# Kernel optimization log

Measured on AMD Instinct MI355X. Metric: run time of the kernel, lower is better.

Reference implementation:

```python
import jax, jax.numpy as jnp
import numpy as np

B = 32768
PASSES = 4

# mask layout: (batch, digit, row, col), values in {0,1}

def _to_lines(m, d):
    """Reorder so the last axis enumerates the 9 cells of a line and axis -2 the 9 lines."""
    if d == 'h':
        return m                      # lines = rows, cells = cols
    if d == 'v':
        return jnp.swapaxes(m, 2, 3)  # lines = cols, cells = rows
    b = m.shape[0]                    # lines = 3x3 boxes
    return m.reshape(b, 9, 3, 3, 3, 3).transpose(0, 1, 2, 4, 3, 5).reshape(b, 9, 9, 9)

_from_lines = _to_lines  # all three reorderings are self-inverse


def filter_line(m, d):
    """SudokuFilterHVBox: remove a solved cell's digit from all other cells in its line."""
    l = _to_lines(m, d)
    cnt = l.sum(axis=1, keepdims=True)                 # candidates per cell
    solved = l * (cnt == 1).astype(l.dtype)            # one-hot solved cells
    other = solved.sum(axis=-1, keepdims=True) - solved  # same digit solved elsewhere in line
    out = l * (other == 0).astype(l.dtype)
    return _from_lines(out, d)


def unique_line(m, d):
    """SudokuUniqueHVBox (hidden single): if a digit fits only one cell in a line, fix it."""
    l = _to_lines(m, d)
    cnt_line = l.sum(axis=-1, keepdims=True)           # per-digit count in the line
    hidden = l * (cnt_line == 1).astype(l.dtype)       # lone placements
    has = hidden.sum(axis=1, keepdims=True) > 0        # cell hosts a hidden single
    out = jnp.where(has, hidden, l)
    return _from_lines(out, d)


def doubles_line(m, d):
    """SudokuDigitsDoubles (naked pair): two identical 2-candidate cells in a line
    eliminate those digits from the rest of the line."""
    l = _to_lines(m, d)                                # (B, d, line, cell)
    cnt = l.sum(axis=1, keepdims=True)
    pm = l * (cnt == 2).astype(l.dtype)                # patterns of 2-candidate cells
    dot = jnp.einsum('bdlc,bdle->blce', pm, pm)        # pattern overlap between cells
    eye = jnp.eye(9, dtype=l.dtype)
    match = (dot == 2).astype(l.dtype) * (1.0 - eye)   # identical pair at another cell
    pairflag = match.sum(-1) > 0                       # (B, line, cell) part of a naked pair
    pair_digit = pm * pairflag[:, None, :, :].astype(l.dtype)
    total_pd = pair_digit.sum(-1, keepdims=True)       # digit belongs to some pair in line
    remove = (total_pd > 0) & (pair_digit == 0)
    out = l * (1.0 - remove.astype(l.dtype))
    return _from_lines(out, d)


def pointing(m, d):
    """SudokuDigitsInOneLineAtBox: if a digit's box candidates lie in one row/col,
    remove that digit from the rest of the row/col outside the box."""
    b = m.shape[0]
    v = m.reshape(b, 9, 3, 3, 3, 3)                    # (B, d, br, ri, bc, ci)
    if d == 'h':
        pres = v.sum(axis=5) > 0                       # (B,d,br,ri,bc) digit in row of box
        nrows = pres.sum(axis=3, keepdims=True)
        point = pres & (nrows == 1)                    # confined to single row within box
        tot = point.sum(axis=4, keepdims=True)         # over bc
        rem = (tot - point) > 0                        # pointing from another box hits us
        out = v * (1.0 - rem[..., None].astype(v.dtype))
    else:
        pres = v.sum(axis=3) > 0                       # (B,d,br,bc,ci) digit in col of box
        ncols = pres.sum(axis=4, keepdims=True)
        point = pres & (ncols == 1)
        tot = point.sum(axis=2, keepdims=True)         # over br
        rem = (tot - point) > 0
        out = v * (1.0 - rem[:, :, :, None, :, :].astype(v.dtype))
    return out.reshape(b, 9, 9, 9)


def _forward_mask(mask):
    for _ in range(PASSES):
        mask = filter_line(mask, 'box')
        mask = pointing(mask, 'h')
        mask = pointing(mask, 'v')
        mask = unique_line(mask, 'h')
        mask = unique_line(mask, 'v')
        mask = unique_line(mask, 'box')
        mask = doubles_line(mask, 'v')   # original code instantiates doubles_h with 'v'
        mask = doubles_line(mask, 'v')
        mask = doubles_line(mask, 'box')
    return mask


def setup_inputs() -> dict:
    key = jax.random.key(0)
    mask = jax.random.randint(key, (B, 9, 9, 9), 0, 2).astype(jnp.float32)
    return {"mask": mask}


def reference(mask):
    out = _forward_mask(mask)
    cnt = out.sum(axis=1)                              # candidates per cell
    solved = jnp.all(cnt == 1, axis=(1, 2))            # (B,) puzzle fully determined
    return (out, solved)
```

## Files before the change

### kernel.cpp

```cpp
#include <hip/hip_runtime.h>
#include <stdint.h>

#define NB 32768
#define NPASS 4
#define FULL27 0x07FFFFFFu
#define NWORDS (NB * 27)


__global__ __launch_bounds__(256)
void pack_kernel(const uint32_t* __restrict__ in, uint32_t* __restrict__ packed) {
    __shared__ uint32_t pool[4][56];
    const int lane = threadIdx.x & 63;
    const int wv = threadIdx.x >> 6;
    const size_t wordBase = (size_t)blockIdx.x * 256 + (size_t)wv * 64;
    const uint32_t* src = in + wordBase * 27;
    #pragma unroll
    for (int i = 0; i < 27; ++i) {
        uint32_t v = src[(size_t)i * 64 + lane];
        unsigned long long m = __ballot(v != 0u);
        if (lane == 0) {
            pool[wv][2 * i]     = (uint32_t)m;
            pool[wv][2 * i + 1] = (uint32_t)(m >> 32);
        }
    }
    __syncthreads();
    const int bit = lane * 27;
    const int di = bit >> 5;
    uint64_t both = (uint64_t)pool[wv][di] | ((uint64_t)pool[wv][di + 1] << 32);
    packed[wordBase + lane] = (uint32_t)(both >> (bit & 31)) & FULL27;
}

__global__ __launch_bounds__(256, 1)
void solve_kernel(const uint32_t* __restrict__ pin, uint32_t* __restrict__ pout,
                  float* __restrict__ solved) {
    int p = blockIdx.x * blockDim.x + threadIdx.x;
    if (p >= NB) return;
    uint32_t bd[9][3];
    {
        const uint32_t* src = pin + (size_t)p * 27;
        #pragma unroll
        for (int i = 0; i < 27; ++i) bd[i / 3][i % 3] = src[i];
    }

    #pragma unroll 1
    for (int pass = 0; pass < NPASS; ++pass) {
        {
            uint32_t on[3] = {0,0,0}, tw[3] = {0,0,0}, fo[3] = {0,0,0};
            #pragma unroll
            for (int d = 0; d < 9; ++d)
                #pragma unroll
                for (int b = 0; b < 3; ++b) {
                    uint32_t c = on[b] & bd[d][b];
                    on[b] ^= bd[d][b];
                    fo[b] |= tw[b] & c;
                    tw[b] ^= c;
                }
            uint32_t ex1[3];
            #pragma unroll
            for (int b = 0; b < 3; ++b) ex1[b] = on[b] & ~tw[b] & ~fo[b];
            #pragma unroll
            for (int d = 0; d < 9; ++d)
                #pragma unroll
                for (int b = 0; b < 3; ++b) {
                    uint32_t s = bd[d][b] & ex1[b];
                    #pragma unroll
                    for (int k = 0; k < 3; ++k) {
                        uint32_t bm = 0x1C0E07u << (3 * k);
                        uint32_t sm = s & bm;
                        uint32_t multi = sm & (sm - 1u);
                        uint32_t keep = (sm == 0u) ? 0xFFFFFFFFu : (~bm | (multi ? 0u : sm));
                        bd[d][b] &= keep;
                    }
                }
        }

        #pragma unroll
        for (int d = 0; d < 9; ++d)
            #pragma unroll
            for (int b = 0; b < 3; ++b) {
                uint32_t w = bd[d][b];
                uint32_t t = (w | (w >> 1) | (w >> 2)) & 0x01249249u;
                uint32_t sum = (t & 0x1FFu) + ((t >> 9) & 0x1FFu) + ((t >> 18) & 0x1FFu);
                uint32_t single = sum & ~(sum >> 1) & 0x49u;
                uint32_t point = t & (single * 0x40201u);
                uint32_t clearm = 0;
                #pragma unroll
                for (int r = 0; r < 3; ++r) {
                    uint32_t pr = (point >> (9 * r)) & 0x1FFu;
                    uint32_t multi = pr & (pr - 1u);
                    uint32_t segkeep = multi ? 0u : pr * 7u;
                    uint32_t rc = pr ? ((0x1FFu & ~segkeep) << (9 * r)) : 0u;
                    clearm |= rc;
                }
                bd[d][b] = w & ~clearm;
            }

        #pragma unroll
        for (int d = 0; d < 9; ++d) {
            uint32_t pnt[3];
            #pragma unroll
            for (int b = 0; b < 3; ++b) {
                uint32_t w = bd[d][b];
                uint32_t q = (w | (w >> 9) | (w >> 18)) & 0x1FFu;
                uint32_t u = (q & 0x49u) + ((q >> 1) & 0x49u) + ((q >> 2) & 0x49u);
                uint32_t single = u & ~(u >> 1) & 0x49u;
                pnt[b] = q & (single * 7u);
            }
            bd[d][0] &= ~((pnt[1] | pnt[2]) * 0x40201u);
            bd[d][1] &= ~((pnt[0] | pnt[2]) * 0x40201u);
            bd[d][2] &= ~((pnt[0] | pnt[1]) * 0x40201u);
        }

        {
            uint32_t hid[9][3];
            uint32_t has[3] = {0,0,0};
            #pragma unroll
            for (int d = 0; d < 9; ++d)
                #pragma unroll
                for (int b = 0; b < 3; ++b) {
                    uint32_t w = bd[d][b], h = 0;
                    #pragma unroll
                    for (int r = 0; r < 3; ++r) {
                        uint32_t x = w & (0x1FFu << (9 * r));
                        h |= (x & (x - 1u)) ? 0u : x;
                    }
                    hid[d][b] = h;
                    has[b] |= h;
                }
            #pragma unroll
            for (int d = 0; d < 9; ++d)
                #pragma unroll
                for (int b = 0; b < 3; ++b)
                    bd[d][b] = (bd[d][b] & ~has[b]) | hid[d][b];
        }

        {
            uint32_t hid[9][3];
            uint32_t has[3] = {0,0,0};
            #pragma unroll
            for (int d = 0; d < 9; ++d) {
                uint32_t h0 = 0, h1 = 0, h2 = 0;
                #pragma unroll
                for (int c = 0; c < 9; ++c) {
                    uint32_t cm = 0x40201u << c;
                    uint32_t a0 = bd[d][0] & cm;
                    uint32_t a1 = bd[d][1] & cm;
                    uint32_t a2 = bd[d][2] & cm;
                    uint32_t cnt = (uint32_t)(__popc(a0) + __popc(a1) + __popc(a2));
                    uint32_t mm = (cnt == 1u) ? 0xFFFFFFFFu : 0u;
                    h0 |= a0 & mm; h1 |= a1 & mm; h2 |= a2 & mm;
                }
                hid[d][0] = h0; hid[d][1] = h1; hid[d][2] = h2;
                has[0] |= h0; has[1] |= h1; has[2] |= h2;
            }
            #pragma unroll
            for (int d = 0; d < 9; ++d)
                #pragma unroll
                for (int b = 0; b < 3; ++b)
                    bd[d][b] = (bd[d][b] & ~has[b]) | hid[d][b];
        }

        {
            uint32_t hid[9][3];
            uint32_t has[3] = {0,0,0};
            #pragma unroll
            for (int d = 0; d < 9; ++d)
                #pragma unroll
                for (int b = 0; b < 3; ++b) {
                    uint32_t w = bd[d][b], h = 0;
                    #pragma unroll
                    for (int k = 0; k < 3; ++k) {
                        uint32_t x = w & (0x1C0E07u << (3 * k));
                        h |= (x & (x - 1u)) ? 0u : x;
                    }
                    hid[d][b] = h;
                    has[b] |= h;
                }
            #pragma unroll
            for (int d = 0; d < 9; ++d)
                #pragma unroll
                for (int b = 0; b < 3; ++b)
                    bd[d][b] = (bd[d][b] & ~has[b]) | hid[d][b];
        }

        #pragma unroll 1
        for (int rep = 0; rep < 2; ++rep) {
            uint32_t on[3] = {0,0,0}, tw[3] = {0,0,0}, fo[3] = {0,0,0};
            #pragma unroll
            for (int d = 0; d < 9; ++d)
                #pragma unroll
                for (int b = 0; b < 3; ++b) {
                    uint32_t c = on[b] & bd[d][b];
                    on[b] ^= bd[d][b];
                    fo[b] |= tw[b] & c;
                    tw[b] ^= c;
                }
            uint32_t ex2[3], Q[9][3], K[9][3];
            #pragma unroll
            for (int b = 0; b < 3; ++b) ex2[b] = tw[b] & ~on[b] & ~fo[b];
            #pragma unroll
            for (int d = 0; d < 9; ++d)
                #pragma unroll
                for (int b = 0; b < 3; ++b) { Q[d][b] = bd[d][b] & ex2[b]; K[d][b] = 0u; }
            #pragma unroll
            for (int d1 = 0; d1 < 9; ++d1)
                #pragma unroll
                for (int d2 = d1 + 1; d2 < 9; ++d2) {
                    uint32_t P0 = Q[d1][0] & Q[d2][0];
                    uint32_t P1 = Q[d1][1] & Q[d2][1];
                    uint32_t P2 = Q[d1][2] & Q[d2][2];
                    uint32_t f0 = (P0 | (P0 >> 9) | (P0 >> 18)) & 0x1FFu;
                    uint32_t f1 = (P1 | (P1 >> 9) | (P1 >> 18)) & 0x1FFu;
                    uint32_t f2 = (P2 | (P2 >> 9) | (P2 >> 18)) & 0x1FFu;
                    uint32_t g0 = ((P0 & (P0 >> 9)) | ((P0 | (P0 >> 9)) & (P0 >> 18))) & 0x1FFu;
                    uint32_t g1 = ((P1 & (P1 >> 9)) | ((P1 | (P1 >> 9)) & (P1 >> 18))) & 0x1FFu;
                    uint32_t g2 = ((P2 & (P2 >> 9)) | ((P2 | (P2 >> 9)) & (P2 >> 18))) & 0x1FFu;
                    uint32_t dup = g0 | g1 | g2 | (f0 & f1) | (f0 & f2) | (f1 & f2);
                    uint32_t em = dup * 0x40201u;
                    uint32_t s0 = P0 & em, s1 = P1 & em, s2 = P2 & em;
                    K[d1][0] |= s0; K[d1][1] |= s1; K[d1][2] |= s2;
                    K[d2][0] |= s0; K[d2][1] |= s1; K[d2][2] |= s2;
                }
            #pragma unroll
            for (int d = 0; d < 9; ++d) {
                uint32_t fold = K[d][0] | K[d][1] | K[d][2];
                uint32_t cols = (fold | (fold >> 9) | (fold >> 18)) & 0x1FFu;
                uint32_t em = cols * 0x40201u;
                #pragma unroll
                for (int b = 0; b < 3; ++b)
                    bd[d][b] = (bd[d][b] & ~em) | K[d][b];
            }
        }

        {
            uint32_t on[3] = {0,0,0}, tw[3] = {0,0,0}, fo[3] = {0,0,0};
            #pragma unroll
            for (int d = 0; d < 9; ++d)
                #pragma unroll
                for (int b = 0; b < 3; ++b) {
                    uint32_t c = on[b] & bd[d][b];
                    on[b] ^= bd[d][b];
                    fo[b] |= tw[b] & c;
                    tw[b] ^= c;
                }
            uint32_t ex2[3], Q[9][3], K[9][3];
            #pragma unroll
            for (int b = 0; b < 3; ++b) ex2[b] = tw[b] & ~on[b] & ~fo[b];
            #pragma unroll
            for (int d = 0; d < 9; ++d)
                #pragma unroll
                for (int b = 0; b < 3; ++b) { Q[d][b] = bd[d][b] & ex2[b]; K[d][b] = 0u; }
            #pragma unroll
            for (int d1 = 0; d1 < 9; ++d1)
                #pragma unroll
                for (int d2 = d1 + 1; d2 < 9; ++d2)
                    #pragma unroll
                    for (int b = 0; b < 3; ++b) {
                        uint32_t P = Q[d1][b] & Q[d2][b];
                        #pragma unroll
                        for (int k = 0; k < 3; ++k) {
                            uint32_t m = P & (0x1C0E07u << (3 * k));
                            uint32_t s = (m & (m - 1u)) ? m : 0u;
                            K[d1][b] |= s; K[d2][b] |= s;
                        }
                    }
            #pragma unroll
            for (int d = 0; d < 9; ++d)
                #pragma unroll
                for (int b = 0; b < 3; ++b)
                    #pragma unroll
                    for (int k = 0; k < 3; ++k) {
                        uint32_t bm = 0x1C0E07u << (3 * k);
                        uint32_t t = K[d][b] & bm;
                        uint32_t mask = t ? (~bm | t) : 0xFFFFFFFFu;
                        bd[d][b] &= mask;
                    }
        }
    }

    {
        uint32_t* dst = pout + (size_t)p * 27;
        #pragma unroll
        for (int i = 0; i < 27; ++i) dst[i] = bd[i / 3][i % 3];
    }
    {
        uint32_t on[3] = {0,0,0}, tw[3] = {0,0,0}, fo[3] = {0,0,0};
        #pragma unroll
        for (int d = 0; d < 9; ++d)
            #pragma unroll
            for (int b = 0; b < 3; ++b) {
                uint32_t c = on[b] & bd[d][b];
                on[b] ^= bd[d][b];
                fo[b] |= tw[b] & c;
                tw[b] ^= c;
            }
        bool ok = ((on[0] & ~tw[0] & ~fo[0]) == FULL27) &&
                  ((on[1] & ~tw[1] & ~fo[1]) == FULL27) &&
                  ((on[2] & ~tw[2] & ~fo[2]) == FULL27);
        solved[p] = ok ? 1.0f : 0.0f;
    }
}

__global__ __launch_bounds__(256)
void expand_kernel(const uint32_t* __restrict__ packed, float4* __restrict__ out4) {
    int tid = blockIdx.x * blockDim.x + threadIdx.x;
    int base = tid * 4;
    int w0 = (int)((unsigned)base / 27u);
    int pos0 = base - w0 * 27;
    uint32_t a = packed[w0];
    int w1 = w0 + 1; if (w1 > NWORDS - 1) w1 = NWORDS - 1;
    uint32_t b = packed[w1];
    float r[4];
    #pragma unroll
    for (int k = 0; k < 4; ++k) {
        int pp = pos0 + k;
        uint32_t word = (pp < 27) ? a : b;
        int sh = (pp < 27) ? pp : pp - 27;
        r[k] = (float)((word >> sh) & 1u);
    }
    out4[tid] = make_float4(r[0], r[1], r[2], r[3]);
}

extern "C" void kernel_launch(void* const* d_in, const int* in_sizes, int n_in,
                              void* d_out, int out_size, void* d_ws, size_t ws_size,
                              hipStream_t stream) {
    const uint32_t* in = (const uint32_t*)d_in[0];
    float* out = (float*)d_out;
    float* solved = out + (size_t)NB * 729;
    uint32_t* packed = (uint32_t*)d_ws;

    pack_kernel<<<NWORDS / 256, 256, 0, stream>>>(in, packed);
    solve_kernel<<<NB / 256, 256, 0, stream>>>(packed, packed, solved);
    expand_kernel<<<(NB * 729 / 4) / 256, 256, 0, stream>>>(packed, (float4*)out);
}
```

Before: 256.3 us.

## Split each puzzle across three threads by band with shared-memory exchange

The solve kernel now gives each puzzle to three threads, one per 3-row band, instead of one. Each thread holds 9 words instead of 27. Column-wise steps (column pointing, column hidden singles, column naked pairs, the solved check) exchange folded per-band summaries through shared memory with __syncthreads. This cuts register pressure and raises parallelism, since the old kernel had only 128 blocks of 256 threads. The cost is extra LDS traffic and block-wide barriers, about 30 KB of shared memory per block, and the same redundant colfold work repeated in each thread.

```diff
diff --git a/kernel.cpp b/kernel.cpp
--- a/kernel.cpp
+++ b/kernel.cpp
@@ -30,274 +30,250 @@
     packed[wordBase + lane] = (uint32_t)(both >> (bit & 31)) & FULL27;
 }
 
-__global__ __launch_bounds__(256, 1)
+__device__ __forceinline__ uint32_t colfold(uint32_t w) {
+    return (w | (w >> 9) | (w >> 18)) & 0x1FFu;
+}
+__device__ __forceinline__ uint32_t colmaj2(uint32_t w) {
+    return ((w & (w >> 9)) | ((w | (w >> 9)) & (w >> 18))) & 0x1FFu;
+}
+
+__global__ __launch_bounds__(192, 1)
 void solve_kernel(const uint32_t* __restrict__ pin, uint32_t* __restrict__ pout,
                   float* __restrict__ solved) {
-    int p = blockIdx.x * blockDim.x + threadIdx.x;
-    if (p >= NB) return;
-    uint32_t bd[9][3];
+    __shared__ uint32_t exA[3][36][64];
+    __shared__ uint32_t exB[3][9][64];
+    const int lane = threadIdx.x & 63;
+    const int band = threadIdx.x >> 6;
+    const int bo1 = band == 2 ? 0 : band + 1;
+    const int bo2 = band == 0 ? 2 : band - 1;
+    const int p = blockIdx.x * 64 + lane;
+
+    uint32_t bd[9];
     {
-        const uint32_t* src = pin + (size_t)p * 27;
-        #pragma unroll
-        for (int i = 0; i < 27; ++i) bd[i / 3][i % 3] = src[i];
+        const uint32_t* src = pin + (size_t)p * 27 + band;
+        #pragma unroll
+        for (int d = 0; d < 9; ++d) bd[d] = src[d * 3];
     }
 
     #pragma unroll 1
     for (int pass = 0; pass < NPASS; ++pass) {
         {
-            uint32_t on[3] = {0,0,0}, tw[3] = {0,0,0}, fo[3] = {0,0,0};
-            #pragma unroll
-            for (int d = 0; d < 9; ++d)
-                #pragma unroll
-                for (int b = 0; b < 3; ++b) {
-                    uint32_t c = on[b] & bd[d][b];
-                    on[b] ^= bd[d][b];
-                    fo[b] |= tw[b] & c;
-                    tw[b] ^= c;
-                }
-            uint32_t ex1[3];
-            #pragma unroll
-            for (int b = 0; b < 3; ++b) ex1[b] = on[b] & ~tw[b] & ~fo[b];
-            #pragma unroll
-            for (int d = 0; d < 9; ++d)
-                #pragma unroll
-                for (int b = 0; b < 3; ++b) {
-                    uint32_t s = bd[d][b] & ex1[b];
+            uint32_t on = 0, tw = 0, fo = 0;
+            #pragma unroll
+            for (int d = 0; d < 9; ++d) {
+                uint32_t c = on & bd[d];
+                on ^= bd[d]; fo |= tw & c; tw ^= c;
+            }
+            uint32_t ex1 = on & ~tw & ~fo;
+            #pragma unroll
+            for (int d = 0; d < 9; ++d) {
+                uint32_t s = bd[d] & ex1;
+                #pragma unroll
+                for (int k = 0; k < 3; ++k) {
+                    uint32_t bm = 0x1C0E07u << (3 * k);
+                    uint32_t sm = s & bm;
+                    uint32_t multi = sm & (sm - 1u);
+                    uint32_t keep = (sm == 0u) ? 0xFFFFFFFFu : (~bm | (multi ? 0u : sm));
+                    bd[d] &= keep;
+                }
+            }
+        }
+
+        #pragma unroll
+        for (int d = 0; d < 9; ++d) {
+            uint32_t w = bd[d];
+            uint32_t t = (w | (w >> 1) | (w >> 2)) & 0x01249249u;
+            uint32_t sum = (t & 0x1FFu) + ((t >> 9) & 0x1FFu) + ((t >> 18) & 0x1FFu);
+            uint32_t single = sum & ~(sum >> 1) & 0x49u;
+            uint32_t point = t & (single * 0x40201u);
+            uint32_t clearm = 0;
+            #pragma unroll
+            for (int r = 0; r < 3; ++r) {
+                uint32_t pr = (point >> (9 * r)) & 0x1FFu;
+                uint32_t multi = pr & (pr - 1u);
+                uint32_t segkeep = multi ? 0u : pr * 7u;
+                uint32_t rc = pr ? ((0x1FFu & ~segkeep) << (9 * r)) : 0u;
+                clearm |= rc;
+            }
+            bd[d] = w & ~clearm;
+        }
+
+        #pragma unroll
+        for (int d = 0; d < 9; ++d) {
+            uint32_t w = bd[d];
+            uint32_t q = colfold(w);
+            uint32_t u = (q & 0x49u) + ((q >> 1) & 0x49u) + ((q >> 2) & 0x49u);
+            uint32_t single = u & ~(u >> 1) & 0x49u;
+            exA[band][d][lane] = q & (single * 7u);
+        }
+        __syncthreads();
+        #pragma unroll
+        for (int d = 0; d < 9; ++d) {
+            uint32_t o = exA[bo1][d][lane] | exA[bo2][d][lane];
+            bd[d] &= ~(o * 0x40201u);
+        }
+
+        {
+            uint32_t hid[9], has = 0;
+            #pragma unroll
+            for (int d = 0; d < 9; ++d) {
+                uint32_t w = bd[d], h = 0;
+                #pragma unroll
+                for (int r = 0; r < 3; ++r) {
+                    uint32_t x = w & (0x1FFu << (9 * r));
+                    h |= (x & (x - 1u)) ? 0u : x;
+                }
+                hid[d] = h; has |= h;
+            }
+            #pragma unroll
+            for (int d = 0; d < 9; ++d) bd[d] = (bd[d] & ~has) | hid[d];
+        }
+
+        {
+            #pragma unroll
+            for (int d = 0; d < 9; ++d) {
+                uint32_t w = bd[d];
+                exB[band][d][lane] = colfold(w) | (colmaj2(w) << 9);
+            }
+            __syncthreads();
+            uint32_t hid[9], has = 0;
+            #pragma unroll
+            for (int d = 0; d < 9; ++d) {
+                uint32_t w = bd[d];
+                uint32_t q0 = colfold(w), m0 = colmaj2(w);
+                uint32_t ea = exB[bo1][d][lane], eb = exB[bo2][d][lane];
+                uint32_t qa = ea & 0x1FFu, ma = ea >> 9;
+                uint32_t qb = eb & 0x1FFu, mb = eb >> 9;
+                uint32_t ge2 = m0 | ma | mb | (q0 & qa) | (q0 & qb) | (qa & qb);
+                uint32_t ex1c = (q0 | qa | qb) & ~ge2;
+                hid[d] = w & ((ex1c & q0) * 0x40201u);
+                has |= hid[d];
+            }
+            #pragma unroll
+            for (int d = 0; d < 9; ++d) bd[d] = (bd[d] & ~has) | hid[d];
+        }
+
+        {
+            uint32_t hid[9], has = 0;
+            #pragma unroll
+            for (int d = 0; d < 9; ++d) {
+                uint32_t w = bd[d], h = 0;
+                #pragma unroll
+                for (int k = 0; k < 3; ++k) {
+                    uint32_t x = w & (0x1C0E07u << (3 * k));
+                    h |= (x & (x - 1u)) ? 0u : x;
+                }
+                hid[d] = h; has |= h;
+            }
+            #pragma unroll
+            for (int d = 0; d < 9; ++d) bd[d] = (bd[d] & ~has) | hid[d];
+        }
+
+        #pragma unroll 1
+        for (int rep = 0; rep < 2; ++rep) {
+            uint32_t on = 0, tw = 0, fo = 0;
+            #pragma unroll
+            for (int d = 0; d < 9; ++d) {
+                uint32_t c = on & bd[d];
+                on ^= bd[d]; fo |= tw & c; tw ^= c;
+            }
+            uint32_t ex2 = tw & ~on & ~fo;
+            uint32_t Q[9], K[9];
+            #pragma unroll
+            for (int d = 0; d < 9; ++d) { Q[d] = bd[d] & ex2; K[d] = 0u; }
+            {
+                int s = 0;
+                #pragma unroll
+                for (int d1 = 0; d1 < 9; ++d1)
+                    #pragma unroll
+                    for (int d2 = d1 + 1; d2 < 9; ++d2) {
+                        uint32_t P = Q[d1] & Q[d2];
+                        exA[band][s][lane] = colfold(P) | (colmaj2(P) << 9);
+                        ++s;
+                    }
+            }
+            __syncthreads();
+            {
+                int s = 0;
+                #pragma unroll
+                for (int d1 = 0; d1 < 9; ++d1)
+                    #pragma unroll
+                    for (int d2 = d1 + 1; d2 < 9; ++d2) {
+                        uint32_t P = Q[d1] & Q[d2];
+                        uint32_t f0 = colfold(P), g0 = colmaj2(P);
+                        uint32_t ea = exA[bo1][s][lane], eb = exA[bo2][s][lane];
+                        uint32_t fa = ea & 0x1FFu, ga = ea >> 9;
+                        uint32_t fb = eb & 0x1FFu, gb = eb >> 9;
+                        uint32_t dup = g0 | ga | gb | (f0 & fa) | (f0 & fb) | (fa & fb);
+                        uint32_t sK = P & (dup * 0x40201u);
+                        K[d1] |= sK; K[d2] |= sK;
+                        ++s;
+                    }
+            }
+            #pragma unroll
+            for (int d = 0; d < 9; ++d) exB[band][d][lane] = colfold(K[d]);
+            __syncthreads();
+            #pragma unroll
+            for (int d = 0; d < 9; ++d) {
+                uint32_t cols = colfold(K[d]) | exB[bo1][d][lane] | exB[bo2][d][lane];
+                uint32_t em = cols * 0x40201u;
+                bd[d] = (bd[d] & ~em) | K[d];
+            }
+        }
+
+        {
+            uint32_t on = 0, tw = 0, fo = 0;
+            #pragma unroll
+            for (int d = 0; d < 9; ++d) {
+                uint32_t c = on & bd[d];
+                on ^= bd[d]; fo |= tw & c; tw ^= c;
+            }
+            uint32_t ex2 = tw & ~on & ~fo;
+            uint32_t Q[9], K[9];
+            #pragma unroll
+            for (int d = 0; d < 9; ++d) { Q[d] = bd[d] & ex2; K[d] = 0u; }
+            #pragma unroll
+            for (int d1 = 0; d1 < 9; ++d1)
+                #pragma unroll
+                for (int d2 = d1 + 1; d2 < 9; ++d2) {
+                    uint32_t P = Q[d1] & Q[d2];
                     #pragma unroll
                     for (int k = 0; k < 3; ++k) {
-                        uint32_t bm = 0x1C0E07u << (3 * k);
-                        uint32_t sm = s & bm;
-                        uint32_t multi = sm & (sm - 1u);
-                        uint32_t keep = (sm == 0u) ? 0xFFFFFFFFu : (~bm | (multi ? 0u : sm));
-                        bd[d][b] &= keep;
+                        uint32_t m = P & (0x1C0E07u << (3 * k));
+                        uint32_t s = (m & (m - 1u)) ? m : 0u;
+                        K[d1] |= s; K[d2] |= s;
                     }
                 }
-        }
-
-        #pragma unroll
-        for (int d = 0; d < 9; ++d)
-            #pragma unroll
-            for (int b = 0; b < 3; ++b) {
-                uint32_t w = bd[d][b];
-                uint32_t t = (w | (w >> 1) | (w >> 2)) & 0x01249249u;
-                uint32_t sum = (t & 0x1FFu) + ((t >> 9) & 0x1FFu) + ((t >> 18) & 0x1FFu);
-                uint32_t single = sum & ~(sum >> 1) & 0x49u;
-                uint32_t point = t & (single * 0x40201u);
-                uint32_t clearm = 0;
-                #pragma unroll
-                for (int r = 0; r < 3; ++r) {
-                    uint32_t pr = (point >> (9 * r)) & 0x1FFu;
-                    uint32_t multi = pr & (pr - 1u);
-                    uint32_t segkeep = multi ? 0u : pr * 7u;
-                    uint32_t rc = pr ? ((0x1FFu & ~segkeep) << (9 * r)) : 0u;
-                    clearm |= rc;
-                }
-                bd[d][b] = w & ~clearm;
-            }
-
+            #pragma unroll
+            for (int d = 0; d < 9; ++d)
+                #pragma unroll
+                for (int k = 0; k < 3; ++k) {
+                    uint32_t bm = 0x1C0E07u << (3 * k);
+                    uint32_t t = K[d] & bm;
+                    uint32_t mask = t ? (~bm | t) : 0xFFFFFFFFu;
+                    bd[d] &= mask;
+                }
+        }
+    }
+
+    {
+        uint32_t* dst = pout + (size_t)p * 27 + band;
+        #pragma unroll
+        for (int d = 0; d < 9; ++d) dst[d * 3] = bd[d];
+    }
+    {
+        uint32_t on = 0, tw = 0, fo = 0;
         #pragma unroll
         for (int d = 0; d < 9; ++d) {
-            uint32_t pnt[3];
-            #pragma unroll
-            for (int b = 0; b < 3; ++b) {
-                uint32_t w = bd[d][b];
-                uint32_t q = (w | (w >> 9) | (w >> 18)) & 0x1FFu;
-                uint32_t u = (q & 0x49u) + ((q >> 1) & 0x49u) + ((q >> 2) & 0x49u);
-                uint32_t single = u & ~(u >> 1) & 0x49u;
-                pnt[b] = q & (single * 7u);
-            }
-            bd[d][0] &= ~((pnt[1] | pnt[2]) * 0x40201u);
-            bd[d][1] &= ~((pnt[0] | pnt[2]) * 0x40201u);
-            bd[d][2] &= ~((pnt[0] | pnt[1]) * 0x40201u);
-        }
-
-        {
-            uint32_t hid[9][3];
-            uint32_t has[3] = {0,0,0};
-            #pragma unroll
-            for (int d = 0; d < 9; ++d)
-                #pragma unroll
-                for (int b = 0; b < 3; ++b) {
-                    uint32_t w = bd[d][b], h = 0;
-                    #pragma unroll
-                    for (int r = 0; r < 3; ++r) {
-                        uint32_t x = w & (0x1FFu << (9 * r));
-                        h |= (x & (x - 1u)) ? 0u : x;
-                    }
-                    hid[d][b] = h;
-                    has[b] |= h;
-                }
-            #pragma unroll
-            for (int d = 0; d < 9; ++d)
-                #pragma unroll
-                for (int b = 0; b < 3; ++b)
-                    bd[d][b] = (bd[d][b] & ~has[b]) | hid[d][b];
-        }
-
-        {
-            uint32_t hid[9][3];
-            uint32_t has[3] = {0,0,0};
-            #pragma unroll
-            for (int d = 0; d < 9; ++d) {
-                uint32_t h0 = 0, h1 = 0, h2 = 0;
-                #pragma unroll
-                for (int c = 0; c < 9; ++c) {
-                    uint32_t cm = 0x40201u << c;
-                    uint32_t a0 = bd[d][0] & cm;
-                    uint32_t a1 = bd[d][1] & cm;
-                    uint32_t a2 = bd[d][2] & cm;
-                    uint32_t cnt = (uint32_t)(__popc(a0) + __popc(a1) + __popc(a2));
-                    uint32_t mm = (cnt == 1u) ? 0xFFFFFFFFu : 0u;
-                    h0 |= a0 & mm; h1 |= a1 & mm; h2 |= a2 & mm;
-                }
-                hid[d][0] = h0; hid[d][1] = h1; hid[d][2] = h2;
-                has[0] |= h0; has[1] |= h1; has[2] |= h2;
-            }
-            #pragma unroll
-            for (int d = 0; d < 9; ++d)
-                #pragma unroll
-                for (int b = 0; b < 3; ++b)
-                    bd[d][b] = (bd[d][b] & ~has[b]) | hid[d][b];
-        }
-
-        {
-            uint32_t hid[9][3];
-            uint32_t has[3] = {0,0,0};
-            #pragma unroll
-            for (int d = 0; d < 9; ++d)
-                #pragma unroll
-                for (int b = 0; b < 3; ++b) {
-                    uint32_t w = bd[d][b], h = 0;
-                    #pragma unroll
-                    for (int k = 0; k < 3; ++k) {
-                        uint32_t x = w & (0x1C0E07u << (3 * k));
-                        h |= (x & (x - 1u)) ? 0u : x;
-                    }
-                    hid[d][b] = h;
-                    has[b] |= h;
-                }
-            #pragma unroll
-            for (int d = 0; d < 9; ++d)
-                #pragma unroll
-                for (int b = 0; b < 3; ++b)
-                    bd[d][b] = (bd[d][b] & ~has[b]) | hid[d][b];
-        }
-
-        #pragma unroll 1
-        for (int rep = 0; rep < 2; ++rep) {
-            uint32_t on[3] = {0,0,0}, tw[3] = {0,0,0}, fo[3] = {0,0,0};
-            #pragma unroll
-            for (int d = 0; d < 9; ++d)
-                #pragma unroll
-                for (int b = 0; b < 3; ++b) {
-                    uint32_t c = on[b] & bd[d][b];
-                    on[b] ^= bd[d][b];
-                    fo[b] |= tw[b] & c;
-                    tw[b] ^= c;
-                }
-            uint32_t ex2[3], Q[9][3], K[9][3];
-            #pragma unroll
-            for (int b = 0; b < 3; ++b) ex2[b] = tw[b] & ~on[b] & ~fo[b];
-            #pragma unroll
-            for (int d = 0; d < 9; ++d)
-                #pragma unroll
-                for (int b = 0; b < 3; ++b) { Q[d][b] = bd[d][b] & ex2[b]; K[d][b] = 0u; }
-            #pragma unroll
-            for (int d1 = 0; d1 < 9; ++d1)
-                #pragma unroll
-                for (int d2 = d1 + 1; d2 < 9; ++d2) {
-                    uint32_t P0 = Q[d1][0] & Q[d2][0];
-                    uint32_t P1 = Q[d1][1] & Q[d2][1];
-                    uint32_t P2 = Q[d1][2] & Q[d2][2];
-                    uint32_t f0 = (P0 | (P0 >> 9) | (P0 >> 18)) & 0x1FFu;
-                    uint32_t f1 = (P1 | (P1 >> 9) | (P1 >> 18)) & 0x1FFu;
-                    uint32_t f2 = (P2 | (P2 >> 9) | (P2 >> 18)) & 0x1FFu;
-                    uint32_t g0 = ((P0 & (P0 >> 9)) | ((P0 | (P0 >> 9)) & (P0 >> 18))) & 0x1FFu;
-                    uint32_t g1 = ((P1 & (P1 >> 9)) | ((P1 | (P1 >> 9)) & (P1 >> 18))) & 0x1FFu;
-                    uint32_t g2 = ((P2 & (P2 >> 9)) | ((P2 | (P2 >> 9)) & (P2 >> 18))) & 0x1FFu;
-                    uint32_t dup = g0 | g1 | g2 | (f0 & f1) | (f0 & f2) | (f1 & f2);
-                    uint32_t em = dup * 0x40201u;
-                    uint32_t s0 = P0 & em, s1 = P1 & em, s2 = P2 & em;
-                    K[d1][0] |= s0; K[d1][1] |= s1; K[d1][2] |= s2;
-                    K[d2][0] |= s0; K[d2][1] |= s1; K[d2][2] |= s2;
-                }
-            #pragma unroll
-            for (int d = 0; d < 9; ++d) {
-                uint32_t fold = K[d][0] | K[d][1] | K[d][2];
-                uint32_t cols = (fold | (fold >> 9) | (fold >> 18)) & 0x1FFu;
-                uint32_t em = cols * 0x40201u;
-                #pragma unroll
-                for (int b = 0; b < 3; ++b)
-                    bd[d][b] = (bd[d][b] & ~em) | K[d][b];
-            }
-        }
-
-        {
-            uint32_t on[3] = {0,0,0}, tw[3] = {0,0,0}, fo[3] = {0,0,0};
-            #pragma unroll
-            for (int d = 0; d < 9; ++d)
-                #pragma unroll
-                for (int b = 0; b < 3; ++b) {
-                    uint32_t c = on[b] & bd[d][b];
-                    on[b] ^= bd[d][b];
-                    fo[b] |= tw[b] & c;
-                    tw[b] ^= c;
-                }
-            uint32_t ex2[3], Q[9][3], K[9][3];
-            #pragma unroll
-            for (int b = 0; b < 3; ++b) ex2[b] = tw[b] & ~on[b] & ~fo[b];
-            #pragma unroll
-            for (int d = 0; d < 9; ++d)
-                #pragma unroll
-                for (int b = 0; b < 3; ++b) { Q[d][b] = bd[d][b] & ex2[b]; K[d][b] = 0u; }
-            #pragma unroll
-            for (int d1 = 0; d1 < 9; ++d1)
-                #pragma unroll
-                for (int d2 = d1 + 1; d2 < 9; ++d2)
-                    #pragma unroll
-                    for (int b = 0; b < 3; ++b) {
-                        uint32_t P = Q[d1][b] & Q[d2][b];
-                        #pragma unroll
-                        for (int k = 0; k < 3; ++k) {
-                            uint32_t m = P & (0x1C0E07u << (3 * k));
-                            uint32_t s = (m & (m - 1u)) ? m : 0u;
-                            K[d1][b] |= s; K[d2][b] |= s;
-                        }
-                    }
-            #pragma unroll
-            for (int d = 0; d < 9; ++d)
-                #pragma unroll
-                for (int b = 0; b < 3; ++b)
-                    #pragma unroll
-                    for (int k = 0; k < 3; ++k) {
-                        uint32_t bm = 0x1C0E07u << (3 * k);
-                        uint32_t t = K[d][b] & bm;
-                        uint32_t mask = t ? (~bm | t) : 0xFFFFFFFFu;
-                        bd[d][b] &= mask;
-                    }
-        }
-    }
-
-    {
-        uint32_t* dst = pout + (size_t)p * 27;
-        #pragma unroll
-        for (int i = 0; i < 27; ++i) dst[i] = bd[i / 3][i % 3];
-    }
-    {
-        uint32_t on[3] = {0,0,0}, tw[3] = {0,0,0}, fo[3] = {0,0,0};
-        #pragma unroll
-        for (int d = 0; d < 9; ++d)
-            #pragma unroll
-            for (int b = 0; b < 3; ++b) {
-                uint32_t c = on[b] & bd[d][b];
-                on[b] ^= bd[d][b];
-                fo[b] |= tw[b] & c;
-                tw[b] ^= c;
-            }
-        bool ok = ((on[0] & ~tw[0] & ~fo[0]) == FULL27) &&
-                  ((on[1] & ~tw[1] & ~fo[1]) == FULL27) &&
-                  ((on[2] & ~tw[2] & ~fo[2]) == FULL27);
-        solved[p] = ok ? 1.0f : 0.0f;
+            uint32_t c = on & bd[d];
+            on ^= bd[d]; fo |= tw & c; tw ^= c;
+        }
+        exA[band][0][lane] = ((on & ~tw & ~fo) == FULL27) ? 1u : 0u;
+        __syncthreads();
+        if (band == 0) {
+            uint32_t all = exA[0][0][lane] & exA[1][0][lane] & exA[2][0][lane];
+            solved[p] = all ? 1.0f : 0.0f;
+        }
     }
 }
 
@@ -330,6 +306,6 @@
     uint32_t* packed = (uint32_t*)d_ws;
 
     pack_kernel<<<NWORDS / 256, 256, 0, stream>>>(in, packed);
-    solve_kernel<<<NB / 256, 256, 0, stream>>>(packed, packed, solved);
+    solve_kernel<<<NB / 64, 192, 0, stream>>>(packed, packed, solved);
     expand_kernel<<<(NB * 729 / 4) / 256, 256, 0, stream>>>(packed, (float4*)out);
 }
```

Result: faster. 235.4 us (-8.1%).
